# Performance work log

Hardware: AMD Instinct MI355X
Metric: run time of the kernel (lower is better)

Reference implementation:

```python
import jax, jax.numpy as jnp
import numpy as np

B, D, E, C = 16384, 2048, 16, 64  # batch, feat_dim, num_experts, classes per expert
CLASS_STARTS = np.arange(E, dtype=np.int32) * C  # contiguous equal-size class ranges


def setup_inputs() -> dict:
    key = jax.random.key(0)
    k1, k2, k3, k4, k5 = jax.random.split(key, 5)
    return {
        "features": jax.random.normal(k1, (B, D), dtype=jnp.float32),
        "coarse_w": jax.random.normal(k2, (E, D), dtype=jnp.float32) * 0.02,
        "coarse_b": jax.random.normal(k3, (E,), dtype=jnp.float32) * 0.02,
        "expert_w": jax.random.normal(k4, (E, C, D), dtype=jnp.float32) * 0.02,
        "expert_b": jax.random.normal(k5, (E, C), dtype=jnp.float32) * 0.02,
    }


def reference(features, coarse_w, coarse_b, expert_w, expert_b):
    # coarse router: Linear(feat_dim -> num_experts)
    coarse_output = features @ coarse_w.T + coarse_b          # [B, E]
    expert_id = jnp.argmax(coarse_output, axis=1)             # [B] top-1 routing

    # all-expert heads as one batched GEMM, then select routed expert per sample
    # (same math as gather-by-mask + per-expert Linear + scatter-back loop)
    y_all = jnp.einsum('bd,ecd->bec', features, expert_w) + expert_b  # [B, E, C]
    y = jnp.take_along_axis(y_all, expert_id[:, None, None], axis=1)[:, 0, :]  # [B, C]

    # local_preds: softmax probs of the routed expert (all experts have C = max classes)
    local_preds = jax.nn.softmax(y, axis=1)                   # [B, C]

    # global prediction = local argmax + expert's class-range start
    starts = jnp.asarray(CLASS_STARTS)
    global_preds = (jnp.argmax(y, axis=1) + starts[expert_id]).astype(jnp.float32)  # [B]

    return coarse_output, expert_id, local_preds, global_preds
```

## Files before the change

### kernel.cpp

```cpp
#include <hip/hip_runtime.h>
#include <cstdint>

static constexpr int B_ = 16384;
static constexpr int D_ = 2048;
static constexpr int E_ = 16;
static constexpr int C_ = 64;
static constexpr int KCH = 32;
static constexpr int TR_E = 64;
static constexpr int SK_E = 4;
static constexpr int TR_C = 128;
static constexpr int SK_C = 8;
static constexpr int MAXITEMS = (B_ / TR_E) + E_;

template <int RPT, int CPT, int NC, int TR, int SK, bool FLAT>
__global__ __launch_bounds__(256) void gemm_tile(
    const float* __restrict__ feat, const float* __restrict__ Wall,
    const int* __restrict__ rowList, const int* __restrict__ cnt,
    const int* __restrict__ sched, const int* __restrict__ nItems,
    float* __restrict__ part0,
    float* __restrict__ partRest)
{
  constexpr int FITER = TR / 32;
  constexpr int WSLOTS = NC * 8;
  constexpr int WITER = (WSLOTS + 255) / 256;
  constexpr int CG = NC / CPT;

  __shared__ float fT[KCH * TR];
  __shared__ float wT[KCH * NC];
  __shared__ int rIdx[TR];

  const int tid = threadIdx.x;
  int e, tile, kz;
  if (FLAT) {
    const int b = blockIdx.x;
    kz = b % SK;
    const int item = b / SK;
    if (item >= *nItems) return;
    const int s = sched[item];
    e = s & 255;
    tile = s >> 8;
  } else {
    e = 0;
    tile = blockIdx.x;
    kz = blockIdx.z;
  }
  const int count = cnt ? cnt[e] : B_;

  if (tid < TR) {
    const int slot = tile * TR + tid;
    rIdx[tid] = (slot < count) ? (rowList ? rowList[e * B_ + slot] : slot) : 0;
  }
  __syncthreads();

  unsigned grows[FITER];
  int dcf[FITER], sbf[FITER];
#pragma unroll
  for (int i = 0; i < FITER; ++i) {
    const int idx = i * 256 + tid;
    const int rl = idx >> 3;
    dcf[i] = idx & 7;
    grows[i] = (unsigned)rIdx[rl];
    sbf[i] = (((rl >> 3) ^ dcf[i]) << 3) + (rl & 7);
  }
  int wc[WITER], wdc[WITER], wsb[WITER];
  bool wact[WITER];
#pragma unroll
  for (int i = 0; i < WITER; ++i) {
    const int idx = i * 256 + tid;
    wact[i] = idx < WSLOTS;
    const int c = (idx < WSLOTS) ? (idx >> 3) : 0;
    wc[i] = c;
    wdc[i] = idx & 7;
    wsb[i] = (((c >> 3) ^ (wdc[i] & (NC / 8 - 1))) << 3) + (c & 7);
  }

  const int cg = tid % CG;
  const int rg = tid / CG;

  float acc[RPT][CPT];
#pragma unroll
  for (int r = 0; r < RPT; ++r)
#pragma unroll
    for (int c = 0; c < CPT; ++c) acc[r][c] = 0.f;

  const float* We = Wall + (size_t)e * NC * D_;
  constexpr int KRANGE = D_ / SK;
  constexpr int NCH = KRANGE / KCH;
  const int k0 = kz * KRANGE;

  float4 pf[FITER], pw[WITER];
#pragma unroll
  for (int i = 0; i < FITER; ++i)
    pf[i] = *(const float4*)(feat + (size_t)grows[i] * D_ + k0 + dcf[i] * 4);
#pragma unroll
  for (int i = 0; i < WITER; ++i)
    if (wact[i])
      pw[i] = *(const float4*)(We + (size_t)wc[i] * D_ + k0 + wdc[i] * 4);

  for (int ch = 0; ch < NCH; ++ch) {
#pragma unroll
    for (int i = 0; i < FITER; ++i) {
      float* p = &fT[(dcf[i] * 4) * TR + sbf[i]];
      p[0 * TR] = pf[i].x;
      p[1 * TR] = pf[i].y;
      p[2 * TR] = pf[i].z;
      p[3 * TR] = pf[i].w;
    }
#pragma unroll
    for (int i = 0; i < WITER; ++i)
      if (wact[i]) {
        float* p = &wT[(wdc[i] * 4) * NC + wsb[i]];
        p[0 * NC] = pw[i].x;
        p[1 * NC] = pw[i].y;
        p[2 * NC] = pw[i].z;
        p[3 * NC] = pw[i].w;
      }
    __syncthreads();
    if (ch + 1 < NCH) {
      const int kb = k0 + (ch + 1) * KCH;
#pragma unroll
      for (int i = 0; i < FITER; ++i)
        pf[i] = *(const float4*)(feat + (size_t)grows[i] * D_ + kb + dcf[i] * 4);
#pragma unroll
      for (int i = 0; i < WITER; ++i)
        if (wact[i])
          pw[i] = *(const float4*)(We + (size_t)wc[i] * D_ + kb + wdc[i] * 4);
    }
#pragma unroll
    for (int dd = 0; dd < KCH; ++dd) {
      const int s = dd >> 2;
      const int sw = s & (NC / 8 - 1);
      float a[RPT], bb[CPT];
#pragma unroll
      for (int r4 = 0; r4 < RPT / 4; ++r4) {
        const int col = rg * RPT + r4 * 4;
        const float4 v =
            *(const float4*)&fT[dd * TR + (((col >> 3) ^ s) << 3) + (col & 7)];
        a[r4 * 4 + 0] = v.x;
        a[r4 * 4 + 1] = v.y;
        a[r4 * 4 + 2] = v.z;
        a[r4 * 4 + 3] = v.w;
      }
      if constexpr (CPT >= 4) {
#pragma unroll
        for (int c4 = 0; c4 < CPT / 4; ++c4) {
          const int col = cg * CPT + c4 * 4;
          const float4 v =
              *(const float4*)&wT[dd * NC + (((col >> 3) ^ sw) << 3) + (col & 7)];
          bb[c4 * 4 + 0] = v.x;
          bb[c4 * 4 + 1] = v.y;
          bb[c4 * 4 + 2] = v.z;
          bb[c4 * 4 + 3] = v.w;
        }
      } else {
        const int col = cg * 2;
        const float2 v =
            *(const float2*)&wT[dd * NC + (((col >> 3) ^ sw) << 3) + (col & 7)];
        bb[0] = v.x;
        bb[1] = v.y;
      }
#pragma unroll
      for (int r = 0; r < RPT; ++r)
#pragma unroll
        for (int c = 0; c < CPT; ++c) acc[r][c] += a[r] * bb[c];
    }
    __syncthreads();
  }

  float* pk = kz ? (partRest + (size_t)(kz - 1) * B_ * NC) : part0;
#pragma unroll
  for (int r = 0; r < RPT; ++r) {
    const int lrow = rg * RPT + r;
    const int slot = tile * TR + lrow;
    if (slot < count) {
      const int grow = rIdx[lrow];
      float* dst = pk + (size_t)grow * NC + cg * CPT;
      if constexpr (CPT >= 4) {
#pragma unroll
        for (int c4 = 0; c4 < CPT / 4; ++c4)
          *(float4*)(dst + c4 * 4) =
              make_float4(acc[r][c4 * 4 + 0], acc[r][c4 * 4 + 1],
                          acc[r][c4 * 4 + 2], acc[r][c4 * 4 + 3]);
      } else {
        *(float2*)dst = make_float2(acc[r][0], acc[r][1]);
      }
    }
  }
}

__global__ __launch_bounds__(256) void coarse_finish(
    const float* __restrict__ cpart0, const float* __restrict__ cpartRest,
    const float* __restrict__ cb, float* __restrict__ out0,
    float* __restrict__ out1, int* __restrict__ eidArr, int* __restrict__ cnt,
    int* __restrict__ rowList) {
  __shared__ int lcnt[E_];
  __shared__ int lbase[E_];
  const int tid = threadIdx.x;
  if (tid < E_) lcnt[tid] = 0;
  __syncthreads();
  const int row = blockIdx.x * 256 + tid;

  float v[E_];
#pragma unroll
  for (int j = 0; j < E_; ++j) v[j] = cb[j];
#pragma unroll
  for (int kz = 0; kz < SK_C; ++kz) {
    const float* p = (kz == 0) ? (cpart0 + (size_t)row * E_)
                               : (cpartRest + ((size_t)(kz - 1) * B_ + row) * E_);
#pragma unroll
    for (int j4 = 0; j4 < E_ / 4; ++j4) {
      const float4 t = *(const float4*)(p + j4 * 4);
      v[j4 * 4 + 0] += t.x;
      v[j4 * 4 + 1] += t.y;
      v[j4 * 4 + 2] += t.z;
      v[j4 * 4 + 3] += t.w;
    }
  }
  int best = 0;
  float bv = v[0];
#pragma unroll
  for (int j = 1; j < E_; ++j)
    if (v[j] > bv) { bv = v[j]; best = j; }

  float* o0 = out0 + (size_t)row * E_;
#pragma unroll
  for (int j4 = 0; j4 < E_ / 4; ++j4)
    *(float4*)(o0 + j4 * 4) = make_float4(v[j4 * 4 + 0], v[j4 * 4 + 1],
                                          v[j4 * 4 + 2], v[j4 * 4 + 3]);
  out1[row] = (float)best;
  eidArr[row] = best;

  const int lpos = atomicAdd(&lcnt[best], 1);
  __syncthreads();
  if (tid < E_) lbase[tid] = atomicAdd(&cnt[tid], lcnt[tid]);
  __syncthreads();
  rowList[best * B_ + lbase[best] + lpos] = row;
}

__global__ void make_schedule(const int* __restrict__ cnt,
                              int* __restrict__ sched,
                              int* __restrict__ nItems) {
  __shared__ int tiles[E_];
  __shared__ int offs[E_];
  const int t = threadIdx.x;
  if (t < E_) tiles[t] = (cnt[t] + TR_E - 1) / TR_E;
  __syncthreads();
  if (t == 0) {
    int acc = 0;
    for (int e = 0; e < E_; ++e) {
      offs[e] = acc;
      acc += tiles[e];
    }
    *nItems = acc;
  }
  __syncthreads();
  if (t < E_) {
    const int o = offs[t], n = tiles[t];
    for (int k = 0; k < n; ++k) sched[o + k] = t | (k << 8);
  }
}

__global__ __launch_bounds__(256) void finish_rows(
    const float* __restrict__ ypart0, const float* __restrict__ ypartRest,
    const float* __restrict__ eb, const int* __restrict__ eidArr,
    float* __restrict__ out2, float* __restrict__ out3) {
  const int lane = threadIdx.x & 63;
  const int row = (blockIdx.x * 256 + threadIdx.x) >> 6;
  const int eid = eidArr[row];

  float v = eb[eid * C_ + lane];
  v += ypart0[(size_t)row * C_ + lane];
#pragma unroll
  for (int kz = 1; kz < SK_E; ++kz)
    v += ypartRest[((size_t)(kz - 1) * B_ + row) * C_ + lane];

  float m = v;
#pragma unroll
  for (int off = 32; off; off >>= 1) m = fmaxf(m, __shfl_xor(m, off, 64));
  const float p = __expf(v - m);
  float s = p;
#pragma unroll
  for (int off = 32; off; off >>= 1) s += __shfl_xor(s, off, 64);
  out2[(size_t)row * C_ + lane] = p / s;

  float av = v;
  int ai = lane;
#pragma unroll
  for (int off = 32; off; off >>= 1) {
    const float ov = __shfl_xor(av, off, 64);
    const int oi = __shfl_xor(ai, off, 64);
    if (ov > av || (ov == av && oi < ai)) { av = ov; ai = oi; }
  }
  if (lane == 0) out3[row] = (float)(ai + (eid << 6));
}

extern "C" void kernel_launch(void* const* d_in, const int* in_sizes, int n_in,
                              void* d_out, int out_size, void* d_ws,
                              size_t ws_size, hipStream_t stream) {
  const float* feat = (const float*)d_in[0];
  const float* cw = (const float*)d_in[1];
  const float* cb = (const float*)d_in[2];
  const float* ew = (const float*)d_in[3];
  const float* eb = (const float*)d_in[4];

  float* out0 = (float*)d_out;
  float* out1 = out0 + (size_t)B_ * E_;
  float* out2 = out1 + B_;
  float* out3 = out2 + (size_t)B_ * C_;

  char* ws = (char*)d_ws;
  float* cpartRest = (float*)ws;
  float* ypartRest = cpartRest + (size_t)(SK_C - 1) * B_ * E_;
  int* rowList = (int*)(ypartRest + (size_t)(SK_E - 1) * B_ * C_);
  int* cnt = rowList + (size_t)E_ * B_;
  int* eidArr = cnt + 64;
  int* sched = eidArr + B_;
  int* nItems = sched + 512;

  hipMemsetAsync(cnt, 0, E_ * sizeof(int), stream);

  gemm_tile<4, 2, E_, TR_C, SK_C, false>
      <<<dim3(B_ / TR_C, 1, SK_C), 256, 0, stream>>>(
          feat, cw, nullptr, nullptr, nullptr, nullptr, out0, cpartRest);
  coarse_finish<<<B_ / 256, 256, 0, stream>>>(out0, cpartRest, cb, out0, out1,
                                              eidArr, cnt, rowList);
  make_schedule<<<1, 64, 0, stream>>>(cnt, sched, nItems);
  gemm_tile<4, 4, C_, TR_E, SK_E, true>
      <<<MAXITEMS * SK_E, 256, 0, stream>>>(feat, ew, rowList, cnt, sched,
                                            nItems, out2, ypartRest);
  finish_rows<<<(B_ * 64) / 256, 256, 0, stream>>>(out2, ypartRest, eb, eidArr,
                                                   out2, out3);
}
```

Measured before the change: 298.9 us.

## Retune GEMM tiles, widen expert K-chunk, fold schedule build into coarse finish

The K-chunk size becomes a template parameter. The expert GEMM now stages 64-wide K chunks, so it needs fewer barriers per tile, and the coarse GEMM uses 64-row tiles with 2x2 outputs per thread, giving twice as many blocks. The separate single-block schedule kernel is removed: the last block of coarse_finish, detected with an atomic done counter, builds the expert tile schedule. This drops one launch, at the cost of a threadfence per block and more shared memory in the expert GEMM.

```diff
diff --git a/kernel.cpp b/kernel.cpp
--- a/kernel.cpp
+++ b/kernel.cpp
@@ -5,14 +5,13 @@
 static constexpr int D_ = 2048;
 static constexpr int E_ = 16;
 static constexpr int C_ = 64;
-static constexpr int KCH = 32;
 static constexpr int TR_E = 64;
 static constexpr int SK_E = 4;
-static constexpr int TR_C = 128;
+static constexpr int TR_C = 64;
 static constexpr int SK_C = 8;
 static constexpr int MAXITEMS = (B_ / TR_E) + E_;
 
-template <int RPT, int CPT, int NC, int TR, int SK, bool FLAT>
+template <int RPT, int CPT, int NC, int TR, int SK, int KCH, bool FLAT>
 __global__ __launch_bounds__(256) void gemm_tile(
     const float* __restrict__ feat, const float* __restrict__ Wall,
     const int* __restrict__ rowList, const int* __restrict__ cnt,
@@ -20,10 +19,13 @@
     float* __restrict__ part0,
     float* __restrict__ partRest)
 {
-  constexpr int FITER = TR / 32;
-  constexpr int WSLOTS = NC * 8;
+  constexpr int DCB = KCH / 4;
+  constexpr int FITER = TR * DCB / 256;
+  constexpr int WSLOTS = NC * DCB;
   constexpr int WITER = (WSLOTS + 255) / 256;
   constexpr int CG = NC / CPT;
+  constexpr int RB = TR / 8;
+  constexpr int CB = NC / 8;
 
   __shared__ float fT[KCH * TR];
   __shared__ float wT[KCH * NC];
@@ -57,10 +59,10 @@
 #pragma unroll
   for (int i = 0; i < FITER; ++i) {
     const int idx = i * 256 + tid;
-    const int rl = idx >> 3;
-    dcf[i] = idx & 7;
+    const int rl = idx / DCB;
+    dcf[i] = idx % DCB;
     grows[i] = (unsigned)rIdx[rl];
-    sbf[i] = (((rl >> 3) ^ dcf[i]) << 3) + (rl & 7);
+    sbf[i] = (((rl >> 3) ^ (dcf[i] & (RB - 1))) << 3) + (rl & 7);
   }
   int wc[WITER], wdc[WITER], wsb[WITER];
   bool wact[WITER];
@@ -68,10 +70,10 @@
   for (int i = 0; i < WITER; ++i) {
     const int idx = i * 256 + tid;
     wact[i] = idx < WSLOTS;
-    const int c = (idx < WSLOTS) ? (idx >> 3) : 0;
+    const int c = wact[i] ? (idx / DCB) : 0;
     wc[i] = c;
-    wdc[i] = idx & 7;
-    wsb[i] = (((c >> 3) ^ (wdc[i] & (NC / 8 - 1))) << 3) + (c & 7);
+    wdc[i] = idx % DCB;
+    wsb[i] = (((c >> 3) ^ (wdc[i] & (CB - 1))) << 3) + (c & 7);
   }
 
   const int cg = tid % CG;
@@ -128,25 +130,33 @@
     }
 #pragma unroll
     for (int dd = 0; dd < KCH; ++dd) {
-      const int s = dd >> 2;
-      const int sw = s & (NC / 8 - 1);
+      const int sz = (dd >> 2) & (RB - 1);
+      const int sw = (dd >> 2) & (CB - 1);
       float a[RPT], bb[CPT];
-#pragma unroll
-      for (int r4 = 0; r4 < RPT / 4; ++r4) {
-        const int col = rg * RPT + r4 * 4;
-        const float4 v =
-            *(const float4*)&fT[dd * TR + (((col >> 3) ^ s) << 3) + (col & 7)];
-        a[r4 * 4 + 0] = v.x;
-        a[r4 * 4 + 1] = v.y;
-        a[r4 * 4 + 2] = v.z;
-        a[r4 * 4 + 3] = v.w;
+      if constexpr (RPT >= 4) {
+#pragma unroll
+        for (int r4 = 0; r4 < RPT / 4; ++r4) {
+          const int col = rg * RPT + r4 * 4;
+          const float4 v = *(
+              const float4*)&fT[dd * TR + (((col >> 3) ^ sz) << 3) + (col & 7)];
+          a[r4 * 4 + 0] = v.x;
+          a[r4 * 4 + 1] = v.y;
+          a[r4 * 4 + 2] = v.z;
+          a[r4 * 4 + 3] = v.w;
+        }
+      } else {
+        const int col = rg * 2;
+        const float2 v =
+            *(const float2*)&fT[dd * TR + (((col >> 3) ^ sz) << 3) + (col & 7)];
+        a[0] = v.x;
+        a[1] = v.y;
       }
       if constexpr (CPT >= 4) {
 #pragma unroll
         for (int c4 = 0; c4 < CPT / 4; ++c4) {
           const int col = cg * CPT + c4 * 4;
-          const float4 v =
-              *(const float4*)&wT[dd * NC + (((col >> 3) ^ sw) << 3) + (col & 7)];
+          const float4 v = *(
+              const float4*)&wT[dd * NC + (((col >> 3) ^ sw) << 3) + (col & 7)];
           bb[c4 * 4 + 0] = v.x;
           bb[c4 * 4 + 1] = v.y;
           bb[c4 * 4 + 2] = v.z;
@@ -192,11 +202,14 @@
     const float* __restrict__ cpart0, const float* __restrict__ cpartRest,
     const float* __restrict__ cb, float* __restrict__ out0,
     float* __restrict__ out1, int* __restrict__ eidArr, int* __restrict__ cnt,
-    int* __restrict__ rowList) {
+    int* __restrict__ done, int* __restrict__ rowList, int* __restrict__ sched,
+    int* __restrict__ nItems) {
   __shared__ int lcnt[E_];
   __shared__ int lbase[E_];
+  __shared__ int lastFlag;
   const int tid = threadIdx.x;
   if (tid < E_) lcnt[tid] = 0;
+  if (tid == 0) lastFlag = 0;
   __syncthreads();
   const int row = blockIdx.x * 256 + tid;
 
@@ -220,7 +233,10 @@
   float bv = v[0];
 #pragma unroll
   for (int j = 1; j < E_; ++j)
-    if (v[j] > bv) { bv = v[j]; best = j; }
+    if (v[j] > bv) {
+      bv = v[j];
+      best = j;
+    }
 
   float* o0 = out0 + (size_t)row * E_;
 #pragma unroll
@@ -235,28 +251,27 @@
   if (tid < E_) lbase[tid] = atomicAdd(&cnt[tid], lcnt[tid]);
   __syncthreads();
   rowList[best * B_ + lbase[best] + lpos] = row;
-}
-
-__global__ void make_schedule(const int* __restrict__ cnt,
-                              int* __restrict__ sched,
-                              int* __restrict__ nItems) {
-  __shared__ int tiles[E_];
-  __shared__ int offs[E_];
-  const int t = threadIdx.x;
-  if (t < E_) tiles[t] = (cnt[t] + TR_E - 1) / TR_E;
-  __syncthreads();
-  if (t == 0) {
-    int acc = 0;
-    for (int e = 0; e < E_; ++e) {
-      offs[e] = acc;
-      acc += tiles[e];
-    }
-    *nItems = acc;
-  }
-  __syncthreads();
-  if (t < E_) {
-    const int o = offs[t], n = tiles[t];
-    for (int k = 0; k < n; ++k) sched[o + k] = t | (k << 8);
+
+  __threadfence();
+  if (tid == 0)
+    if (atomicAdd(done, 1) == (int)gridDim.x - 1) lastFlag = 1;
+  __syncthreads();
+  if (lastFlag) {
+    if (tid < E_) lcnt[tid] = (atomicAdd(&cnt[tid], 0) + TR_E - 1) / TR_E;
+    __syncthreads();
+    if (tid == 0) {
+      int a = 0;
+      for (int e = 0; e < E_; ++e) {
+        lbase[e] = a;
+        a += lcnt[e];
+      }
+      *nItems = a;
+    }
+    __syncthreads();
+    if (tid < E_) {
+      const int o = lbase[tid], n = lcnt[tid];
+      for (int k = 0; k < n; ++k) sched[o + k] = tid | (k << 8);
+    }
   }
 }
 
@@ -276,20 +291,23 @@
 
   float m = v;
 #pragma unroll
-  for (int off = 32; off; off >>= 1) m = fmaxf(m, __shfl_xor(m, off, 64));
+  for (int off = 32; off; off >>= 1) m = fmaxf(m, __shfl_xor(m, off));
   const float p = __expf(v - m);
   float s = p;
 #pragma unroll
-  for (int off = 32; off; off >>= 1) s += __shfl_xor(s, off, 64);
+  for (int off = 32; off; off >>= 1) s += __shfl_xor(s, off);
   out2[(size_t)row * C_ + lane] = p / s;
 
   float av = v;
   int ai = lane;
 #pragma unroll
   for (int off = 32; off; off >>= 1) {
-    const float ov = __shfl_xor(av, off, 64);
-    const int oi = __shfl_xor(ai, off, 64);
-    if (ov > av || (ov == av && oi < ai)) { av = ov; ai = oi; }
+    const float ov = __shfl_xor(av, off);
+    const int oi = __shfl_xor(ai, off);
+    if (ov > av || (ov == av && oi < ai)) {
+      av = ov;
+      ai = oi;
+    }
   }
   if (lane == 0) out3[row] = (float)(ai + (eid << 6));
 }
@@ -313,19 +331,20 @@
   float* ypartRest = cpartRest + (size_t)(SK_C - 1) * B_ * E_;
   int* rowList = (int*)(ypartRest + (size_t)(SK_E - 1) * B_ * C_);
   int* cnt = rowList + (size_t)E_ * B_;
+  int* done = cnt + E_;
   int* eidArr = cnt + 64;
   int* sched = eidArr + B_;
   int* nItems = sched + 512;
 
-  hipMemsetAsync(cnt, 0, E_ * sizeof(int), stream);
-
-  gemm_tile<4, 2, E_, TR_C, SK_C, false>
+  hipMemsetAsync(cnt, 0, 256, stream);
+
+  gemm_tile<2, 2, E_, TR_C, SK_C, 32, false>
       <<<dim3(B_ / TR_C, 1, SK_C), 256, 0, stream>>>(
           feat, cw, nullptr, nullptr, nullptr, nullptr, out0, cpartRest);
   coarse_finish<<<B_ / 256, 256, 0, stream>>>(out0, cpartRest, cb, out0, out1,
-                                              eidArr, cnt, rowList);
-  make_schedule<<<1, 64, 0, stream>>>(cnt, sched, nItems);
-  gemm_tile<4, 4, C_, TR_E, SK_E, true>
+                                              eidArr, cnt, done, rowList,
+                                              sched, nItems);
+  gemm_tile<4, 4, C_, TR_E, SK_E, 64, true>
       <<<MAXITEMS * SK_E, 256, 0, stream>>>(feat, ew, rowList, cnt, sched,
                                             nItems, out2, ypartRest);
   finish_rows<<<(B_ * 64) / 256, 256, 0, stream>>>(out2, ypartRest, eb, eidArr,
```

New measurement: 317.3 us. +6.1%, slower.
